# Kernel optimization log

Measured on AMD Instinct MI355X. Metric: run time of the kernel, lower is better.

The kernel has to match this reference:

```python
import jax, jax.numpy as jnp
import numpy as np

T = 1024          # total packed tokens
NUM_SEQS = 4      # ragged batch: 4 sequences
SEQ_LEN = T // NUM_SEQS
D = 2048          # hidden_size
N = 32            # num query heads
K = 8             # num kv heads (GQA)
H = 64            # head_dim
THETA = 500000.0  # rope_theta (Llama-3 style)


def apply_rope(x, positions, theta):
    # x: [T, heads, H]; positions: [T] int32
    h = x.shape[-1]
    half = h // 2
    inv_freq = 1.0 / (theta ** (jnp.arange(half, dtype=jnp.float32) / half))
    freqs = positions.astype(jnp.float32)[:, None] * inv_freq        # [T, half]
    cos = jnp.cos(freqs)[:, None, :]                                 # [T, 1, half]
    sin = jnp.sin(freqs)[:, None, :]
    x1, x2 = jnp.split(x, 2, axis=-1)
    return jnp.concatenate([x1 * cos - x2 * sin, x2 * cos + x1 * sin], axis=-1)


def setup_inputs() -> dict:
    key = jax.random.key(0)
    ks = jax.random.split(key, 5)
    x = jax.random.normal(ks[0], (T, D), dtype=jnp.float32)
    Wq = jax.random.normal(ks[1], (D, N, H), dtype=jnp.float32) * 0.02
    Wk = jax.random.normal(ks[2], (D, K, H), dtype=jnp.float32) * 0.02
    Wv = jax.random.normal(ks[3], (D, K, H), dtype=jnp.float32) * 0.02
    Wo = jax.random.normal(ks[4], (N, H, D), dtype=jnp.float32) * 0.02
    # packed ragged batch: positions restart per sequence, seg_ids mark sequence membership
    positions = jnp.tile(jnp.arange(SEQ_LEN, dtype=jnp.int32), NUM_SEQS)
    seg_ids = jnp.repeat(jnp.arange(NUM_SEQS, dtype=jnp.int32), SEQ_LEN)
    return {"x": x, "Wq": Wq, "Wk": Wk, "Wv": Wv, "Wo": Wo,
            "positions": positions, "seg_ids": seg_ids}


def reference(x, Wq, Wk, Wv, Wo, positions, seg_ids):
    # QKV projections (einsum specs match nnx.Einsum in the module)
    q = jnp.einsum('td,dnh->tnh', x, Wq)          # [T, N, H]
    k = jnp.einsum('td,dkh->tkh', x, Wk)          # [T, K, H]
    v = jnp.einsum('td,dkh->tkh', x, Wv)          # [T, K, H]
    q = apply_rope(q, positions, THETA)
    k = apply_rope(k, positions, THETA)

    # GQA ragged causal attention over packed tokens (equivalent to paged
    # attention over a cache containing exactly these sequences' K/V).
    G = N // K                                    # query heads per kv head
    qg = q.reshape(T, K, G, H)
    scale = 1.0 / jnp.sqrt(jnp.asarray(H, dtype=jnp.float32))
    scores = jnp.einsum('tkgh,skh->kgts', qg, k) * scale   # [K, G, T, T]

    tok = jnp.arange(T)
    mask = (seg_ids[:, None] == seg_ids[None, :]) & (tok[:, None] >= tok[None, :])
    scores = jnp.where(mask[None, None, :, :], scores, jnp.asarray(-1e30, scores.dtype))
    attn = jax.nn.softmax(scores, axis=-1)

    out = jnp.einsum('kgts,skh->tkgh', attn, v).reshape(T, N, H)
    o = jnp.einsum('tnh,nhd->td', out, Wo)        # [T, D]
    return o
```

## Files before the change

kernel.cpp:

```cpp
#include <hip/hip_runtime.h>
#include <hip/hip_bf16.h>
#include <math.h>

#define T_TOK   1024
#define D_DIM   2048
#define NQ      32
#define KHEADS  8
#define HD      64
#define NSEQ    4
#define SEQLEN  256

typedef __attribute__((ext_vector_type(8))) short bf16x8;
typedef __attribute__((ext_vector_type(4))) float f32x4;

__device__ __forceinline__ void glds16(const void* g, void* l) {
  __builtin_amdgcn_global_load_lds(
      (const __attribute__((address_space(1))) void*)g,
      (__attribute__((address_space(3))) void*)l, 16, 0, 0);
}

__device__ __forceinline__ void tcast_body(
    const float* __restrict__ W, __hip_bfloat16* __restrict__ Wt, int N,
    int bx, int by, float (*t)[33]) {
  const int n0 = bx * 32, k0 = by * 32;
  const int ty = threadIdx.x >> 5, tx = threadIdx.x & 31;
#pragma unroll
  for (int r = ty; r < 32; r += 8) t[r][tx] = W[(size_t)(k0 + r) * N + n0 + tx];
  __syncthreads();
#pragma unroll
  for (int r = ty; r < 32; r += 8)
    Wt[(size_t)(n0 + r) * 2048 + k0 + tx] = __float2bfloat16(t[tx][r]);
}

__global__ __launch_bounds__(256) void prep(
    const float* __restrict__ x,
    const float* __restrict__ Wq, const float* __restrict__ Wk,
    const float* __restrict__ Wv, const float* __restrict__ Wo,
    __hip_bfloat16* __restrict__ xb, __hip_bfloat16* __restrict__ Wt) {
  __shared__ float t[32][33];
  const int b = blockIdx.x;
  if (b < 2048) {
    int i = b * 256 + threadIdx.x;
    float4 v = ((const float4*)x)[i];
    ushort4 o;
    __hip_bfloat16 h0 = __float2bfloat16(v.x); o.x = reinterpret_cast<ushort&>(h0);
    __hip_bfloat16 h1 = __float2bfloat16(v.y); o.y = reinterpret_cast<ushort&>(h1);
    __hip_bfloat16 h2 = __float2bfloat16(v.z); o.z = reinterpret_cast<ushort&>(h2);
    __hip_bfloat16 h3 = __float2bfloat16(v.w); o.w = reinterpret_cast<ushort&>(h3);
    *(ushort4*)((ushort*)xb + (size_t)i * 4) = o;
  } else if (b < 6144) {
    int r = b - 2048; tcast_body(Wq, Wt, 2048, r & 63, r >> 6, t);
  } else if (b < 7168) {
    int r = b - 6144; tcast_body(Wk, Wt + (size_t)2048 * 2048, 512, r & 15, r >> 4, t);
  } else if (b < 8192) {
    int r = b - 7168; tcast_body(Wv, Wt + (size_t)2560 * 2048, 512, r & 15, r >> 4, t);
  } else {
    int r = b - 8192; tcast_body(Wo, Wt + (size_t)3072 * 2048, 2048, r & 63, r >> 6, t);
  }
}

__global__ __launch_bounds__(256) void gemm_bf16(
    const ushort* __restrict__ A, const ushort* __restrict__ Bt,
    float* __restrict__ C, int N, int Kd) {
  __shared__ ushort As[2][64 * 64];
  __shared__ ushort Bs[2][64 * 64];
  const int tid = threadIdx.x;
  const int lane = tid & 63;
  const int w = tid >> 6;
  const int wr = w >> 1, wc = w & 1;
  const int brow = blockIdx.y * 64, bcol = blockIdx.x * 64;

  const int srow = lane >> 3;
  const int skc  = ((lane & 7) ^ (lane >> 3)) * 8;

  const int fr = lane & 15;
  const int fg = lane >> 4;

  const ushort* A0 = A + (size_t)brow * Kd;
  const ushort* B0 = Bt + (size_t)bcol * Kd;
  const int nt = Kd >> 6;

  f32x4 acc[2][2] = {};

#pragma unroll
  for (int h = 0; h < 2; ++h) {
    int g = w * 2 + h;
    glds16(&A0[(size_t)(g * 8 + srow) * Kd + skc], &As[0][g * 512]);
    glds16(&B0[(size_t)(g * 8 + srow) * Kd + skc], &Bs[0][g * 512]);
  }
  __syncthreads();

  int cur = 0;
  for (int t = 0; t < nt; ++t) {
    if (t + 1 < nt) {
      int k0 = (t + 1) << 6;
#pragma unroll
      for (int h = 0; h < 2; ++h) {
        int g = w * 2 + h;
        glds16(&A0[(size_t)(g * 8 + srow) * Kd + k0 + skc], &As[cur ^ 1][g * 512]);
        glds16(&B0[(size_t)(g * 8 + srow) * Kd + k0 + skc], &Bs[cur ^ 1][g * 512]);
      }
    }
#pragma unroll
    for (int kk = 0; kk < 2; ++kk) {
      const int cc = ((kk * 4 + fg) ^ (fr & 7)) * 8;
      bf16x8 a[2], b[2];
#pragma unroll
      for (int fi = 0; fi < 2; ++fi)
        a[fi] = *(const bf16x8*)&As[cur][(wr * 32 + fi * 16 + fr) * 64 + cc];
#pragma unroll
      for (int fj = 0; fj < 2; ++fj)
        b[fj] = *(const bf16x8*)&Bs[cur][(wc * 32 + fj * 16 + fr) * 64 + cc];
#pragma unroll
      for (int fi = 0; fi < 2; ++fi)
#pragma unroll
        for (int fj = 0; fj < 2; ++fj)
          acc[fi][fj] = __builtin_amdgcn_mfma_f32_16x16x32_bf16(
              a[fi], b[fj], acc[fi][fj], 0, 0, 0);
    }
    __syncthreads();
    cur ^= 1;
  }

  const int cr0 = brow + wr * 32 + (lane >> 4) * 4;
  const int cc0 = bcol + wc * 32 + fr;
#pragma unroll
  for (int fi = 0; fi < 2; ++fi)
#pragma unroll
    for (int fj = 0; fj < 2; ++fj)
#pragma unroll
      for (int r = 0; r < 4; ++r)
        C[(size_t)(cr0 + fi * 16 + r) * N + cc0 + fj * 16] = acc[fi][fj][r];
}

__global__ __launch_bounds__(256) void attn_kernel(
    const float* __restrict__ qkv, __hip_bfloat16* __restrict__ out_bf) {
  __shared__ float ks_t[64][65];
  __shared__ float qs[4][2][8][64];
  __shared__ float pb[4][8][64];

  const int c  = blockIdx.x;
  const int kn = blockIdx.y;
  const int s  = blockIdx.z;
  const int tid = threadIdx.x;
  const int w = tid >> 6, lane = tid & 63;
  const int n = kn * 4 + w;
  const int r0s[2] = {c * 8, 248 - c * 8};

  const float L2T = 18.931568569324174f / 32.f;

  {
    const int i = lane & 31;
    const bool lo = lane < 32;
    const float inv = exp2f(-(float)i * L2T);
#pragma unroll
    for (int ss = 0; ss < 2; ++ss)
#pragma unroll
      for (int rr = 0; rr < 8; ++rr) {
        const float* qrow = &qkv[(size_t)(s * 256 + r0s[ss] + rr) * 3072 + n * 64];
        float a = qrow[i], b = qrow[i + 32];
        float sn, cs;
        __sincosf((float)(r0s[ss] + rr) * inv, &sn, &cs);
        qs[w][ss][rr][lane] = (lo ? a * cs - b * sn : b * cs + a * sn) * 0.125f;
      }
  }

  const int kc4 = (tid & 15) * 4;
  const int kii = kc4 & 31;
  const bool klo = kc4 < 32;
  float kinv[4];
#pragma unroll
  for (int j = 0; j < 4; ++j) kinv[j] = exp2f(-(float)(kii + j) * L2T);

  float m[2][8], l[2][8], acc[2][8];
#pragma unroll
  for (int ss = 0; ss < 2; ++ss)
#pragma unroll
    for (int rr = 0; rr < 8; ++rr) { m[ss][rr] = -1e30f; l[ss][rr] = 0.f; acc[ss][rr] = 0.f; }

  const int ntiles = (r0s[1] >> 6) + 1;
  for (int tile = 0; tile < ntiles; ++tile) {
    const int j0 = tile * 64;
    __syncthreads();
#pragma unroll
    for (int p = 0; p < 4; ++p) {
      const int ik = (tid >> 4) + p * 16;
      const float* krow = &qkv[(size_t)(s * 256 + j0 + ik) * 3072 + 2048 + kn * 64];
      const float4 a4 = *(const float4*)&krow[kii];
      const float4 b4 = *(const float4*)&krow[kii + 32];
      const float av[4] = {a4.x, a4.y, a4.z, a4.w};
      const float bv[4] = {b4.x, b4.y, b4.z, b4.w};
      const float pos = (float)(j0 + ik);
#pragma unroll
      for (int j = 0; j < 4; ++j) {
        float sn, cs;
        __sincosf(pos * kinv[j], &sn, &cs);
        ks_t[kc4 + j][ik] = klo ? av[j] * cs - bv[j] * sn : bv[j] * cs + av[j] * sn;
      }
    }
    __syncthreads();

    const float* vb = &qkv[(size_t)(s * 256 + j0) * 3072 + 2560 + kn * 64 + lane];

#pragma unroll
    for (int ss = 0; ss < 2; ++ss) {
      const int r0 = r0s[ss];
      if (j0 > r0 + 7) continue;

      float sj[8] = {0.f, 0.f, 0.f, 0.f, 0.f, 0.f, 0.f, 0.f};
      for (int d = 0; d < 64; d += 4) {
        float k0v = ks_t[d + 0][lane], k1v = ks_t[d + 1][lane];
        float k2v = ks_t[d + 2][lane], k3v = ks_t[d + 3][lane];
#pragma unroll
        for (int rr = 0; rr < 8; ++rr) {
          float4 qv = *(const float4*)&qs[w][ss][rr][d];
          sj[rr] = fmaf(qv.x, k0v, fmaf(qv.y, k1v, fmaf(qv.z, k2v, fmaf(qv.w, k3v, sj[rr]))));
        }
      }
      float corr[8];
#pragma unroll
      for (int rr = 0; rr < 8; ++rr) {
        float sv = (j0 + lane <= r0 + rr) ? sj[rr] : -1e30f;
        float tmax = sv;
#pragma unroll
        for (int off = 1; off < 64; off <<= 1) tmax = fmaxf(tmax, __shfl_xor(tmax, off));
        float mnew = fmaxf(m[ss][rr], tmax);
        float p = __expf(sv - mnew);
        float ps = p;
#pragma unroll
        for (int off = 1; off < 64; off <<= 1) ps += __shfl_xor(ps, off);
        corr[rr] = __expf(m[ss][rr] - mnew);
        l[ss][rr] = l[ss][rr] * corr[rr] + ps;
        m[ss][rr] = mnew;
        pb[w][rr][lane] = p;
      }
#pragma unroll
      for (int rr = 0; rr < 8; ++rr) acc[ss][rr] *= corr[rr];

      for (int jj = 0; jj < 64; jj += 4) {
        float v0 = vb[(size_t)(jj + 0) * 3072];
        float v1 = vb[(size_t)(jj + 1) * 3072];
        float v2 = vb[(size_t)(jj + 2) * 3072];
        float v3 = vb[(size_t)(jj + 3) * 3072];
#pragma unroll
        for (int rr = 0; rr < 8; ++rr) {
          const float4 pv = *(const float4*)&pb[w][rr][jj];
          acc[ss][rr] = fmaf(pv.x, v0, fmaf(pv.y, v1, fmaf(pv.z, v2, fmaf(pv.w, v3, acc[ss][rr]))));
        }
      }
    }
  }

#pragma unroll
  for (int ss = 0; ss < 2; ++ss)
#pragma unroll
    for (int rr = 0; rr < 8; ++rr)
      out_bf[(size_t)(s * 256 + r0s[ss] + rr) * 2048 + n * 64 + lane] =
          __float2bfloat16(acc[ss][rr] / l[ss][rr]);
}

extern "C" void kernel_launch(void* const* d_in, const int* in_sizes, int n_in,
                              void* d_out, int out_size, void* d_ws, size_t ws_size,
                              hipStream_t stream) {
  const float* x  = (const float*)d_in[0];
  const float* Wq = (const float*)d_in[1];
  const float* Wk = (const float*)d_in[2];
  const float* Wv = (const float*)d_in[3];
  const float* Wo = (const float*)d_in[4];

  float* qkv = (float*)d_ws;
  __hip_bfloat16* xb = (__hip_bfloat16*)(qkv + (size_t)T_TOK * 3072);
  __hip_bfloat16* Wt = xb + (size_t)T_TOK * 2048;

  prep<<<12288, 256, 0, stream>>>(x, Wq, Wk, Wv, Wo, xb, Wt);

  gemm_bf16<<<dim3(48, 16), 256, 0, stream>>>((const ushort*)xb, (const ushort*)Wt,
                                              qkv, 3072, 2048);

  attn_kernel<<<dim3(16, KHEADS, NSEQ), 256, 0, stream>>>(qkv, xb);

  gemm_bf16<<<dim3(32, 16), 256, 0, stream>>>(
      (const ushort*)xb, (const ushort*)(Wt + (size_t)3072 * 2048),
      (float*)d_out, 2048, 2048);
}
```

Baseline: 197.1 us.

## Widen weight transpose-cast tiles and share V loads across both query row groups

The weight transpose/cast in prep now uses 32x128 tiles with float4 loads and ushort4 stores, which cuts the block count and makes global accesses wider. In attention, the row-sum reduction is deferred: each lane keeps a partial sum that is shuffle-reduced once at the end instead of per tile. V rows are loaded once per tile and applied to both row groups, halving the strided global V reads. The cost is a larger shared-memory tile and a bigger pb buffer, which may lower occupancy.

```diff
diff --git a/kernel.cpp b/kernel.cpp
--- a/kernel.cpp
+++ b/kernel.cpp
@@ -19,17 +19,36 @@
       (__attribute__((address_space(3))) void*)l, 16, 0, 0);
 }
 
-__device__ __forceinline__ void tcast_body(
+__device__ __forceinline__ ushort bf16u(float f) {
+  __hip_bfloat16 h = __float2bfloat16(f);
+  return reinterpret_cast<ushort&>(h);
+}
+
+__device__ __forceinline__ void tcast2_body(
     const float* __restrict__ W, __hip_bfloat16* __restrict__ Wt, int N,
-    int bx, int by, float (*t)[33]) {
-  const int n0 = bx * 32, k0 = by * 32;
-  const int ty = threadIdx.x >> 5, tx = threadIdx.x & 31;
-#pragma unroll
-  for (int r = ty; r < 32; r += 8) t[r][tx] = W[(size_t)(k0 + r) * N + n0 + tx];
+    int bx, int by, float (*t32)[129]) {
+  const int n0 = bx * 128, k0 = by * 32;
+  const int tid = threadIdx.x;
+  const int rr = tid >> 5, q = tid & 31;
+#pragma unroll
+  for (int p = 0; p < 4; ++p) {
+    int r = rr + p * 8;
+    float4 v = *(const float4*)&W[(size_t)(k0 + r) * N + n0 + q * 4];
+    t32[r][q * 4 + 0] = v.x; t32[r][q * 4 + 1] = v.y;
+    t32[r][q * 4 + 2] = v.z; t32[r][q * 4 + 3] = v.w;
+  }
   __syncthreads();
-#pragma unroll
-  for (int r = ty; r < 32; r += 8)
-    Wt[(size_t)(n0 + r) * 2048 + k0 + tx] = __float2bfloat16(t[tx][r]);
+  const int nr = tid >> 3, c = tid & 7;
+#pragma unroll
+  for (int p = 0; p < 4; ++p) {
+    int n = nr + p * 32;
+    ushort4 u;
+    u.x = bf16u(t32[c * 4 + 0][n]);
+    u.y = bf16u(t32[c * 4 + 1][n]);
+    u.z = bf16u(t32[c * 4 + 2][n]);
+    u.w = bf16u(t32[c * 4 + 3][n]);
+    *(ushort4*)((ushort*)Wt + (size_t)(n0 + n) * 2048 + k0 + c * 4) = u;
+  }
 }
 
 __global__ __launch_bounds__(256) void prep(
@@ -37,25 +56,21 @@
     const float* __restrict__ Wq, const float* __restrict__ Wk,
     const float* __restrict__ Wv, const float* __restrict__ Wo,
     __hip_bfloat16* __restrict__ xb, __hip_bfloat16* __restrict__ Wt) {
-  __shared__ float t[32][33];
+  __shared__ float t32[32][129];
   const int b = blockIdx.x;
   if (b < 2048) {
     int i = b * 256 + threadIdx.x;
     float4 v = ((const float4*)x)[i];
-    ushort4 o;
-    __hip_bfloat16 h0 = __float2bfloat16(v.x); o.x = reinterpret_cast<ushort&>(h0);
-    __hip_bfloat16 h1 = __float2bfloat16(v.y); o.y = reinterpret_cast<ushort&>(h1);
-    __hip_bfloat16 h2 = __float2bfloat16(v.z); o.z = reinterpret_cast<ushort&>(h2);
-    __hip_bfloat16 h3 = __float2bfloat16(v.w); o.w = reinterpret_cast<ushort&>(h3);
+    ushort4 o = {bf16u(v.x), bf16u(v.y), bf16u(v.z), bf16u(v.w)};
     *(ushort4*)((ushort*)xb + (size_t)i * 4) = o;
-  } else if (b < 6144) {
-    int r = b - 2048; tcast_body(Wq, Wt, 2048, r & 63, r >> 6, t);
-  } else if (b < 7168) {
-    int r = b - 6144; tcast_body(Wk, Wt + (size_t)2048 * 2048, 512, r & 15, r >> 4, t);
-  } else if (b < 8192) {
-    int r = b - 7168; tcast_body(Wv, Wt + (size_t)2560 * 2048, 512, r & 15, r >> 4, t);
+  } else if (b < 3072) {
+    int r = b - 2048; tcast2_body(Wq, Wt, 2048, r & 15, r >> 4, t32);
+  } else if (b < 3328) {
+    int r = b - 3072; tcast2_body(Wk, Wt + (size_t)2048 * 2048, 512, r & 3, r >> 2, t32);
+  } else if (b < 3584) {
+    int r = b - 3328; tcast2_body(Wv, Wt + (size_t)2560 * 2048, 512, r & 3, r >> 2, t32);
   } else {
-    int r = b - 8192; tcast_body(Wo, Wt + (size_t)3072 * 2048, 2048, r & 63, r >> 6, t);
+    int r = b - 3584; tcast2_body(Wo, Wt + (size_t)3072 * 2048, 2048, r & 15, r >> 4, t32);
   }
 }
 
@@ -137,7 +152,7 @@
     const float* __restrict__ qkv, __hip_bfloat16* __restrict__ out_bf) {
   __shared__ float ks_t[64][65];
   __shared__ float qs[4][2][8][64];
-  __shared__ float pb[4][8][64];
+  __shared__ float pb[4][2][8][64];
 
   const int c  = blockIdx.x;
   const int kn = blockIdx.y;
@@ -172,11 +187,11 @@
 #pragma unroll
   for (int j = 0; j < 4; ++j) kinv[j] = exp2f(-(float)(kii + j) * L2T);
 
-  float m[2][8], l[2][8], acc[2][8];
+  float m[2][8], lp[2][8], acc[2][8];
 #pragma unroll
   for (int ss = 0; ss < 2; ++ss)
 #pragma unroll
-    for (int rr = 0; rr < 8; ++rr) { m[ss][rr] = -1e30f; l[ss][rr] = 0.f; acc[ss][rr] = 0.f; }
+    for (int rr = 0; rr < 8; ++rr) { m[ss][rr] = -1e30f; lp[ss][rr] = 0.f; acc[ss][rr] = 0.f; }
 
   const int ntiles = (r0s[1] >> 6) + 1;
   for (int tile = 0; tile < ntiles; ++tile) {
@@ -200,13 +215,12 @@
     }
     __syncthreads();
 
-    const float* vb = &qkv[(size_t)(s * 256 + j0) * 3072 + 2560 + kn * 64 + lane];
+    const bool act0 = (j0 <= r0s[0] + 7);
 
 #pragma unroll
     for (int ss = 0; ss < 2; ++ss) {
+      if (ss == 0 && !act0) continue;
       const int r0 = r0s[ss];
-      if (j0 > r0 + 7) continue;
-
       float sj[8] = {0.f, 0.f, 0.f, 0.f, 0.f, 0.f, 0.f, 0.f};
       for (int d = 0; d < 64; d += 4) {
         float k0v = ks_t[d + 0][lane], k1v = ks_t[d + 1][lane];
@@ -217,7 +231,6 @@
           sj[rr] = fmaf(qv.x, k0v, fmaf(qv.y, k1v, fmaf(qv.z, k2v, fmaf(qv.w, k3v, sj[rr]))));
         }
       }
-      float corr[8];
 #pragma unroll
       for (int rr = 0; rr < 8; ++rr) {
         float sv = (j0 + lane <= r0 + rr) ? sj[rr] : -1e30f;
@@ -226,37 +239,45 @@
         for (int off = 1; off < 64; off <<= 1) tmax = fmaxf(tmax, __shfl_xor(tmax, off));
         float mnew = fmaxf(m[ss][rr], tmax);
         float p = __expf(sv - mnew);
-        float ps = p;
-#pragma unroll
-        for (int off = 1; off < 64; off <<= 1) ps += __shfl_xor(ps, off);
-        corr[rr] = __expf(m[ss][rr] - mnew);
-        l[ss][rr] = l[ss][rr] * corr[rr] + ps;
+        float corr = __expf(m[ss][rr] - mnew);
+        lp[ss][rr] = lp[ss][rr] * corr + p;
         m[ss][rr] = mnew;
-        pb[w][rr][lane] = p;
-      }
-#pragma unroll
-      for (int rr = 0; rr < 8; ++rr) acc[ss][rr] *= corr[rr];
-
-      for (int jj = 0; jj < 64; jj += 4) {
-        float v0 = vb[(size_t)(jj + 0) * 3072];
-        float v1 = vb[(size_t)(jj + 1) * 3072];
-        float v2 = vb[(size_t)(jj + 2) * 3072];
-        float v3 = vb[(size_t)(jj + 3) * 3072];
+        acc[ss][rr] *= corr;
+        pb[w][ss][rr][lane] = p;
+      }
+    }
+
+    const float* vb = &qkv[(size_t)(s * 256 + j0) * 3072 + 2560 + kn * 64 + lane];
+    for (int jj = 0; jj < 64; jj += 4) {
+      float v0 = vb[(size_t)(jj + 0) * 3072];
+      float v1 = vb[(size_t)(jj + 1) * 3072];
+      float v2 = vb[(size_t)(jj + 2) * 3072];
+      float v3 = vb[(size_t)(jj + 3) * 3072];
+      if (act0) {
 #pragma unroll
         for (int rr = 0; rr < 8; ++rr) {
-          const float4 pv = *(const float4*)&pb[w][rr][jj];
-          acc[ss][rr] = fmaf(pv.x, v0, fmaf(pv.y, v1, fmaf(pv.z, v2, fmaf(pv.w, v3, acc[ss][rr]))));
+          const float4 pv = *(const float4*)&pb[w][0][rr][jj];
+          acc[0][rr] = fmaf(pv.x, v0, fmaf(pv.y, v1, fmaf(pv.z, v2, fmaf(pv.w, v3, acc[0][rr]))));
         }
       }
+#pragma unroll
+      for (int rr = 0; rr < 8; ++rr) {
+        const float4 pv = *(const float4*)&pb[w][1][rr][jj];
+        acc[1][rr] = fmaf(pv.x, v0, fmaf(pv.y, v1, fmaf(pv.z, v2, fmaf(pv.w, v3, acc[1][rr]))));
+      }
     }
   }
 
 #pragma unroll
   for (int ss = 0; ss < 2; ++ss)
 #pragma unroll
-    for (int rr = 0; rr < 8; ++rr)
+    for (int rr = 0; rr < 8; ++rr) {
+      float ls = lp[ss][rr];
+#pragma unroll
+      for (int off = 1; off < 64; off <<= 1) ls += __shfl_xor(ls, off);
       out_bf[(size_t)(s * 256 + r0s[ss] + rr) * 2048 + n * 64 + lane] =
-          __float2bfloat16(acc[ss][rr] / l[ss][rr]);
+          __float2bfloat16(acc[ss][rr] * (1.f / ls));
+    }
 }
 
 extern "C" void kernel_launch(void* const* d_in, const int* in_sizes, int n_in,
@@ -272,7 +293,7 @@
   __hip_bfloat16* xb = (__hip_bfloat16*)(qkv + (size_t)T_TOK * 3072);
   __hip_bfloat16* Wt = xb + (size_t)T_TOK * 2048;
 
-  prep<<<12288, 256, 0, stream>>>(x, Wq, Wk, Wv, Wo, xb, Wt);
+  prep<<<4608, 256, 0, stream>>>(x, Wq, Wk, Wv, Wo, xb, Wt);
 
   gemm_bf16<<<dim3(48, 16), 256, 0, stream>>>((const ushort*)xb, (const ushort*)Wt,
                                               qkv, 3072, 2048);
```

After: 365.0 us. +85.2%, slower.
